# Kernel tuning notes

Hardware: AMD Instinct MI355X
Metric: run time of the kernel (lower is better)

## Reference

```python
import jax, jax.numpy as jnp
import numpy as np

CH = 128
MID = CH // 4  # 32
B, H, W = 16, 128, 128


def _phi(x):
    # elu(x) + 1 (alpha=1)
    return jax.nn.elu(x) + 1.0


def setup_inputs() -> dict:
    key = jax.random.key(0)
    ks = jax.random.split(key, 6)
    x = jax.random.normal(ks[0], (B, CH, H, W), dtype=jnp.float32)
    Wq = jax.random.normal(ks[1], (MID, CH), dtype=jnp.float32) * 0.05
    Wk = jax.random.normal(ks[2], (MID, CH), dtype=jnp.float32) * 0.05
    Wv = jax.random.normal(ks[3], (MID, CH), dtype=jnp.float32) * 0.05
    Wout = jax.random.normal(ks[4], (CH, MID), dtype=jnp.float32) * 0.05
    gamma = jnp.ones((CH,), dtype=jnp.float32)
    beta = jnp.zeros((CH,), dtype=jnp.float32)
    return {"x": x, "Wq": Wq, "Wk": Wk, "Wv": Wv, "Wout": Wout,
            "gamma": gamma, "beta": beta}


def reference(x, Wq, Wk, Wv, Wout, gamma, beta):
    b, c, h, w = x.shape
    n = h * w
    xf = x.reshape(b, c, n)                      # [B, C, N]
    # 1x1 convs == channel matmuls
    Q = _phi(jnp.einsum('mc,bcn->bmn', Wq, xf))  # [B, M, N]
    K = _phi(jnp.einsum('mc,bcn->bmn', Wk, xf))  # [B, M, N]
    V = jnp.einsum('mc,bcn->bmn', Wv, xf)        # [B, M, N]
    # KV-first linear attention
    KV = jnp.einsum('bmn,bvn->bmv', K, V)        # [B, M, M]
    out = jnp.einsum('bmv,bvn->bmn', KV, Q) / (n + 1e-6)  # [B, M, N]
    Ks = jnp.sum(K, axis=-1, keepdims=True)      # [B, M, 1]
    denom = jnp.sum(Q * Ks, axis=1, keepdims=True) + 1e-6  # [B, 1, N]
    out = out / denom
    # output 1x1 conv
    y = jnp.einsum('cm,bmn->bcn', Wout, out).reshape(b, c, h, w)
    # BatchNorm2d (training-mode forward: batch statistics, biased var, eps=1e-5)
    mean = jnp.mean(y, axis=(0, 2, 3), keepdims=True)
    var = jnp.var(y, axis=(0, 2, 3), keepdims=True)
    y = (y - mean) * jax.lax.rsqrt(var + 1e-5)
    y = y * gamma[None, :, None, None] + beta[None, :, None, None]
    return y
```

## Files before the change

### kernel.cpp

```cpp
#include <hip/hip_runtime.h>

#define BB 16
#define CC 128
#define MM 32
#define NN 16384

#define WS_KV     0
#define WS_KS     16384
#define WS_SQ     16896
#define WS_QQ     17408
#define WS_YSUM   33792
#define WS_YSQ    33920
#define WS_ACCEND 34048
#define WS_W2     34304

typedef __bf16 bf16x8 __attribute__((ext_vector_type(8)));
typedef __bf16 bf16x4 __attribute__((ext_vector_type(4)));
typedef float  f32x16 __attribute__((ext_vector_type(16)));

union B8 { bf16x8 v8; bf16x4 v4[2]; };

__device__ __forceinline__ float phi_f(float z) {
    return z > 0.f ? z + 1.f : __expf(z);
}

__device__ __forceinline__ void lds_barrier() {
    asm volatile("s_waitcnt lgkmcnt(0)" ::: "memory");
    __builtin_amdgcn_sched_barrier(0);
    __builtin_amdgcn_s_barrier();
    __builtin_amdgcn_sched_barrier(0);
}

__global__ void zero_kernel(float* ws) {
    const int i = blockIdx.x * 256 + threadIdx.x;
    if (i < (WS_ACCEND / 4)) {
        float4 z; z.x = 0.f; z.y = 0.f; z.z = 0.f; z.w = 0.f;
        ((float4*)ws)[i] = z;
    }
}

__global__ __launch_bounds__(256) void projmfma_kernel(
    const float* __restrict__ x,
    const float* __restrict__ Wq, const float* __restrict__ Wk,
    const float* __restrict__ Wv,
    float* ws, float* __restrict__ qout)
{
    __shared__ __align__(16) char smem[55296];
    __bf16* Xh  = (__bf16*)smem;
    __bf16* Xl  = (__bf16*)(smem + 17408);
    __bf16* ktH = (__bf16*)(smem + 34816);
    __bf16* ktL = (__bf16*)(smem + 39936);
    __bf16* vtH = (__bf16*)(smem + 45056);
    __bf16* vtL = (__bf16*)(smem + 50176);

    const int b = blockIdx.y;
    const int t = threadIdx.x;
    const int w = t >> 6;
    const int l = t & 63;
    const int g = l >> 5;
    const int ln31 = l & 31;

    bf16x8 wh[8], wl[8];
    if (w < 3) {
        const float* Wm = (w == 0) ? Wq : (w == 1) ? Wk : Wv;
        const float* wr = Wm + ln31 * CC;
        #pragma unroll
        for (int kt = 0; kt < 8; ++kt) {
            const int k0 = 16 * kt + 8 * g;
            #pragma unroll
            for (int j = 0; j < 8; ++j) {
                const float f = wr[k0 + j];
                const __bf16 h = (__bf16)f;
                wh[kt][j] = h;
                wl[kt][j] = (__bf16)(f - (float)h);
            }
        }
    }

    f32x16 kvA, ksA;
    bf16x8 ones;
    #pragma unroll
    for (int i = 0; i < 16; ++i) { kvA[i] = 0.f; ksA[i] = 0.f; }
    #pragma unroll
    for (int j = 0; j < 8; ++j) ones[j] = (__bf16)1.0f;

    const int px = t & 31;
    const int cb = t >> 5;

    const float* xbase = x + (size_t)b * CC * NN + (blockIdx.x << 9) + px;

    float xbuf[16];
    #pragma unroll
    for (int j = 0; j < 16; ++j)
        xbuf[j] = xbase[(size_t)(cb * 16 + j) * NN];
    {
        __bf16 hbuf[16], lbuf[16];
        #pragma unroll
        for (int j = 0; j < 16; ++j) {
            const float f = xbuf[j];
            const __bf16 h = (__bf16)f;
            hbuf[j] = h;
            lbuf[j] = (__bf16)(f - (float)h);
        }
        *(bf16x8*)&Xh[px * 136 + cb * 16]     = *(bf16x8*)&hbuf[0];
        *(bf16x8*)&Xh[px * 136 + cb * 16 + 8] = *(bf16x8*)&hbuf[8];
        *(bf16x8*)&Xl[px * 136 + cb * 16]     = *(bf16x8*)&lbuf[0];
        *(bf16x8*)&Xl[px * 136 + cb * 16 + 8] = *(bf16x8*)&lbuf[8];
    }
    lds_barrier();

    for (int tile = 0; tile < 16; ++tile) {
        const int cur = tile & 1;
        const int n0 = (blockIdx.x << 9) + (tile << 5);

        if (tile < 15) {
            const float* xp = xbase + ((tile + 1) << 5);
            #pragma unroll
            for (int j = 0; j < 16; ++j)
                xbuf[j] = xp[(size_t)(cb * 16 + j) * NN];
        }

        f32x16 acc;
        if (w < 3) {
            #pragma unroll
            for (int i = 0; i < 16; ++i) acc[i] = 0.f;
            const __bf16* xh = Xh + cur * 4352 + ln31 * 136;
            const __bf16* xl = Xl + cur * 4352 + ln31 * 136;
            #pragma unroll
            for (int kt = 0; kt < 8; ++kt) {
                const int k0 = 16 * kt + 8 * g;
                const bf16x8 bh = *(const bf16x8*)&xh[k0];
                const bf16x8 bl = *(const bf16x8*)&xl[k0];
                acc = __builtin_amdgcn_mfma_f32_32x32x16_bf16(wh[kt], bh, acc, 0, 0, 0);
                acc = __builtin_amdgcn_mfma_f32_32x32x16_bf16(wh[kt], bl, acc, 0, 0, 0);
                acc = __builtin_amdgcn_mfma_f32_32x32x16_bf16(wl[kt], bh, acc, 0, 0, 0);
            }
        } else if (tile > 0) {
            const int pbuf = (cur ^ 1) * 1280;
            const __bf16* khp = ktH + pbuf + ln31 * 40;
            const __bf16* klp = ktL + pbuf + ln31 * 40;
            const __bf16* vhp = vtH + pbuf + ln31 * 40;
            const __bf16* vlp = vtL + pbuf + ln31 * 40;
            #pragma unroll
            for (int s = 0; s < 2; ++s) {
                const int k0 = s * 16 + g * 8;
                const bf16x8 akh = *(const bf16x8*)&khp[k0];
                const bf16x8 akl = *(const bf16x8*)&klp[k0];
                const bf16x8 bvh = *(const bf16x8*)&vhp[k0];
                const bf16x8 bvl = *(const bf16x8*)&vlp[k0];
                kvA = __builtin_amdgcn_mfma_f32_32x32x16_bf16(akh, bvh, kvA, 0, 0, 0);
                kvA = __builtin_amdgcn_mfma_f32_32x32x16_bf16(akh, bvl, kvA, 0, 0, 0);
                kvA = __builtin_amdgcn_mfma_f32_32x32x16_bf16(akl, bvh, kvA, 0, 0, 0);
                ksA = __builtin_amdgcn_mfma_f32_32x32x16_bf16(akh, ones, ksA, 0, 0, 0);
                ksA = __builtin_amdgcn_mfma_f32_32x32x16_bf16(akl, ones, ksA, 0, 0, 0);
            }
        }

        if (w == 0) {
            float* qp = qout + (size_t)b * CC * NN + n0 + ln31;
            #pragma unroll
            for (int i = 0; i < 16; ++i) {
                const int r = (i & 3) + 8 * (i >> 2) + 4 * g;
                qp[(size_t)r * NN] = phi_f(acc[i]);
            }
        } else if (w == 1) {
            __bf16* kh = ktH + cur * 1280;
            __bf16* kl = ktL + cur * 1280;
            #pragma unroll
            for (int i = 0; i < 16; ++i) {
                const int r = (i & 3) + 8 * (i >> 2) + 4 * g;
                const float f = phi_f(acc[i]);
                const __bf16 h = (__bf16)f;
                kh[r * 40 + ln31] = h;
                kl[r * 40 + ln31] = (__bf16)(f - (float)h);
            }
        } else if (w == 2) {
            __bf16* vh = vtH + cur * 1280;
            __bf16* vl = vtL + cur * 1280;
            #pragma unroll
            for (int i = 0; i < 16; ++i) {
                const int r = (i & 3) + 8 * (i >> 2) + 4 * g;
                const float f = acc[i];
                const __bf16 h = (__bf16)f;
                vh[r * 40 + ln31] = h;
                vl[r * 40 + ln31] = (__bf16)(f - (float)h);
            }
        }

        if (tile < 15) {
            const int nxt = cur ^ 1;
            __bf16 hbuf[16], lbuf[16];
            #pragma unroll
            for (int j = 0; j < 16; ++j) {
                const float f = xbuf[j];
                const __bf16 h = (__bf16)f;
                hbuf[j] = h;
                lbuf[j] = (__bf16)(f - (float)h);
            }
            *(bf16x8*)&Xh[nxt * 4352 + px * 136 + cb * 16]     = *(bf16x8*)&hbuf[0];
            *(bf16x8*)&Xh[nxt * 4352 + px * 136 + cb * 16 + 8] = *(bf16x8*)&hbuf[8];
            *(bf16x8*)&Xl[nxt * 4352 + px * 136 + cb * 16]     = *(bf16x8*)&lbuf[0];
            *(bf16x8*)&Xl[nxt * 4352 + px * 136 + cb * 16 + 8] = *(bf16x8*)&lbuf[8];
        }

        lds_barrier();
    }

    if (w == 3) {
        const int pbuf = 1280;
        const __bf16* khp = ktH + pbuf + ln31 * 40;
        const __bf16* klp = ktL + pbuf + ln31 * 40;
        const __bf16* vhp = vtH + pbuf + ln31 * 40;
        const __bf16* vlp = vtL + pbuf + ln31 * 40;
        #pragma unroll
        for (int s = 0; s < 2; ++s) {
            const int k0 = s * 16 + g * 8;
            const bf16x8 akh = *(const bf16x8*)&khp[k0];
            const bf16x8 akl = *(const bf16x8*)&klp[k0];
            const bf16x8 bvh = *(const bf16x8*)&vhp[k0];
            const bf16x8 bvl = *(const bf16x8*)&vlp[k0];
            kvA = __builtin_amdgcn_mfma_f32_32x32x16_bf16(akh, bvh, kvA, 0, 0, 0);
            kvA = __builtin_amdgcn_mfma_f32_32x32x16_bf16(akh, bvl, kvA, 0, 0, 0);
            kvA = __builtin_amdgcn_mfma_f32_32x32x16_bf16(akl, bvh, kvA, 0, 0, 0);
            ksA = __builtin_amdgcn_mfma_f32_32x32x16_bf16(akh, ones, ksA, 0, 0, 0);
            ksA = __builtin_amdgcn_mfma_f32_32x32x16_bf16(akl, ones, ksA, 0, 0, 0);
        }
        float* kvb = ws + WS_KV + (b << 10);
        #pragma unroll
        for (int i = 0; i < 16; ++i) {
            const int r = (i & 3) + 8 * (i >> 2) + 4 * g;
            atomicAdd(&kvb[r * 32 + ln31], kvA[i]);
        }
        if (ln31 == 0) {
            #pragma unroll
            for (int i = 0; i < 16; ++i) {
                const int r = (i & 3) + 8 * (i >> 2) + 4 * g;
                atomicAdd(&ws[WS_KS + (b << 5) + r], ksA[i]);
            }
        }
    }
}

__global__ __launch_bounds__(256) void qq_kernel(const float* qsrc, float* ws) {
    __shared__ __align__(16) char qsm[33792];
    __bf16* Qh = (__bf16*)qsm;
    __bf16* Ql = (__bf16*)(qsm + 16896);
    float*  red   = (float*)qsm;
    float*  sqred = (float*)(qsm + 17408);

    const int b = blockIdx.y;
    const int t = threadIdx.x;
    const int w = t >> 6;
    const int l = t & 63;
    const int g = l >> 5;
    const int ln31 = l & 31;

    const float* ksb = ws + WS_KS + (b << 5);
    const int n = (blockIdx.x << 8) + t;
    const float* qp = qsrc + (size_t)b * CC * NN + n;

    float qa[32];
    #pragma unroll
    for (int m = 0; m < 32; ++m) qa[m] = qp[(size_t)m * NN];

    float denom = 1e-6f;
    #pragma unroll
    for (int m = 0; m < 32; ++m) denom = fmaf(qa[m], ksb[m], denom);
    const float inv = 1.0f / (16384.0f * denom);
    #pragma unroll
    for (int m = 0; m < 32; ++m) qa[m] *= inv;

    #pragma unroll
    for (int m = 0; m < 32; ++m) {
        const __bf16 h = (__bf16)qa[m];
        Qh[m * 264 + t] = h;
        Ql[m * 264 + t] = (__bf16)(qa[m] - (float)h);
    }
    __syncthreads();

    f32x16 qqA, sqA;
    bf16x8 ones;
    #pragma unroll
    for (int i = 0; i < 16; ++i) { qqA[i] = 0.f; sqA[i] = 0.f; }
    #pragma unroll
    for (int j = 0; j < 8; ++j) ones[j] = (__bf16)1.0f;

    #pragma unroll
    for (int sub = 0; sub < 2; ++sub) {
        #pragma unroll
        for (int s = 0; s < 2; ++s) {
            const int k0 = (w << 6) + (sub << 5) + s * 16 + g * 8;
            const bf16x8 ah = *(const bf16x8*)&Qh[ln31 * 264 + k0];
            const bf16x8 al = *(const bf16x8*)&Ql[ln31 * 264 + k0];
            qqA = __builtin_amdgcn_mfma_f32_32x32x16_bf16(ah, ah, qqA, 0, 0, 0);
            qqA = __builtin_amdgcn_mfma_f32_32x32x16_bf16(ah, al, qqA, 0, 0, 0);
            qqA = __builtin_amdgcn_mfma_f32_32x32x16_bf16(al, ah, qqA, 0, 0, 0);
            sqA = __builtin_amdgcn_mfma_f32_32x32x16_bf16(ah, ones, sqA, 0, 0, 0);
            sqA = __builtin_amdgcn_mfma_f32_32x32x16_bf16(al, ones, sqA, 0, 0, 0);
        }
    }
    __syncthreads();

    #pragma unroll
    for (int i = 0; i < 16; ++i) red[t * 17 + i] = qqA[i];
    if (ln31 == 0) {
        #pragma unroll
        for (int i = 0; i < 16; ++i) {
            const int r = (i & 3) + 8 * (i >> 2) + 4 * g;
            sqred[(w << 5) + r] = sqA[i];
        }
    }
    __syncthreads();
    if (t < 64) {
        float* qqb = ws + WS_QQ + (b << 10);
        #pragma unroll
        for (int i = 0; i < 16; ++i) {
            const int r = (i & 3) + 8 * (i >> 2) + 4 * g;
            const float s = red[t*17+i] + red[(t+64)*17+i] + red[(t+128)*17+i] + red[(t+192)*17+i];
            atomicAdd(&qqb[r * 32 + ln31], s);
        }
    }
    if (t < 32) {
        const float s = sqred[t] + sqred[32 + t] + sqred[64 + t] + sqred[96 + t];
        atomicAdd(&ws[WS_SQ + (b << 5) + t], s);
    }
}

__global__ __launch_bounds__(128) void bnstat_kernel(const float* __restrict__ Wout,
                                                     float* ws) {
    const int b = blockIdx.x;
    const int c = threadIdx.x;
    const float* kvb = ws + WS_KV + (b << 10);
    const float* wo  = Wout + (c << 5);
    float w[32];
    #pragma unroll
    for (int v = 0; v < 32; ++v) w[v] = 0.f;
    for (int m = 0; m < 32; ++m) {
        const float wm = wo[m];
        #pragma unroll
        for (int v = 0; v < 32; ++v) w[v] = fmaf(wm, kvb[(m << 5) + v], w[v]);
    }
    float* w2b = ws + WS_W2 + (b << 12) + (c << 5);
    #pragma unroll
    for (int v = 0; v < 32; ++v) w2b[v] = w[v];

    const float* sq = ws + WS_SQ + (b << 5);
    const float* qq = ws + WS_QQ + (b << 10);
    float mb = 0.f;
    #pragma unroll
    for (int v = 0; v < 32; ++v) mb = fmaf(w[v], sq[v], mb);
    float qf = 0.f;
    for (int u = 0; u < 32; ++u) {
        float tacc = 0.f;
        #pragma unroll
        for (int v = 0; v < 32; ++v) tacc = fmaf(qq[(u << 5) + v], w[v], tacc);
        qf = fmaf(w[u], tacc, qf);
    }
    atomicAdd(&ws[WS_YSUM + c], mb);
    atomicAdd(&ws[WS_YSQ + c], qf);
}

__global__ __launch_bounds__(256) void out_kernel(const float* qsrc, const float* ws,
                                                  const float* __restrict__ gamma,
                                                  const float* __restrict__ beta,
                                                  float* out) {
    __shared__ __align__(16) __bf16 Qh[256 * 36];
    __shared__ __align__(16) __bf16 Ql[256 * 36];
    __shared__ float scs[CC];
    __shared__ float bis[CC];

    const int b = blockIdx.y;
    const int t = threadIdx.x;
    const int w = t >> 6;
    const int l = t & 63;
    const int g = l >> 5;
    const int ln31 = l & 31;

    if (t < CC) {
        const float invBN = 1.0f / 262144.0f;
        const float mean = ws[WS_YSUM + t] * invBN;
        const float var  = ws[WS_YSQ + t] * invBN - mean * mean;
        const float s = gamma[t] * rsqrtf(var + 1e-5f);
        scs[t] = s;
        bis[t] = fmaf(-mean, s, beta[t]);
    }

    const int n = (blockIdx.x << 8) + t;
    const float* ksb = ws + WS_KS + (b << 5);

    const float* qp = qsrc + (size_t)b * CC * NN + n;
    float qa[32];
    #pragma unroll
    for (int m = 0; m < 32; ++m) qa[m] = qp[(size_t)m * NN];

    float d0 = 1e-6f;
    #pragma unroll
    for (int m = 0; m < 32; ++m) d0 = fmaf(qa[m], ksb[m], d0);
    const float inv = 1.0f / (16384.0f * d0);
    #pragma unroll
    for (int m = 0; m < 32; ++m) qa[m] *= inv;

    {
        __bf16 qh[32], ql[32];
        #pragma unroll
        for (int m = 0; m < 32; ++m) {
            const __bf16 h = (__bf16)qa[m];
            qh[m] = h;
            ql[m] = (__bf16)(qa[m] - (float)h);
        }
        #pragma unroll
        for (int i = 0; i < 8; ++i) {
            *(bf16x4*)&Qh[t * 36 + i * 4] = *(bf16x4*)&qh[i * 4];
            *(bf16x4*)&Ql[t * 36 + i * 4] = *(bf16x4*)&ql[i * 4];
        }
    }
    __syncthreads();

    const float* w2b = ws + WS_W2 + (b << 12);
    float* ob = out + (size_t)b * CC * NN + (blockIdx.x << 8);

    #pragma unroll
    for (int cb = 0; cb < 4; ++cb) {
        bf16x8 ah[2], al[2];
        #pragma unroll
        for (int kt = 0; kt < 2; ++kt) {
            const float* wp = w2b + (cb * 32 + ln31) * 32 + kt * 16 + g * 8;
            #pragma unroll
            for (int j = 0; j < 8; ++j) {
                const float f = wp[j];
                const __bf16 h = (__bf16)f;
                ah[kt][j] = h;
                al[kt][j] = (__bf16)(f - (float)h);
            }
        }
        #pragma unroll
        for (int pg = 0; pg < 2; ++pg) {
            const int px0 = (w << 6) + (pg << 5);
            f32x16 acc;
            #pragma unroll
            for (int i = 0; i < 16; ++i) acc[i] = 0.f;
            #pragma unroll
            for (int kt = 0; kt < 2; ++kt) {
                const int k0 = kt * 16 + g * 8;
                const __bf16* qhp = &Qh[(px0 + ln31) * 36 + k0];
                const __bf16* qlp = &Ql[(px0 + ln31) * 36 + k0];
                B8 bh, bl;
                bh.v4[0] = *(const bf16x4*)&qhp[0];
                bh.v4[1] = *(const bf16x4*)&qhp[4];
                bl.v4[0] = *(const bf16x4*)&qlp[0];
                bl.v4[1] = *(const bf16x4*)&qlp[4];
                acc = __builtin_amdgcn_mfma_f32_32x32x16_bf16(ah[kt], bh.v8, acc, 0, 0, 0);
                acc = __builtin_amdgcn_mfma_f32_32x32x16_bf16(ah[kt], bl.v8, acc, 0, 0, 0);
                acc = __builtin_amdgcn_mfma_f32_32x32x16_bf16(al[kt], bh.v8, acc, 0, 0, 0);
            }
            #pragma unroll
            for (int i = 0; i < 16; ++i) {
                const int r = (i & 3) + 8 * (i >> 2) + 4 * g;
                const int c = cb * 32 + r;
                const float v = fmaf(scs[c], acc[i], bis[c]);
                __builtin_nontemporal_store(v, &ob[(size_t)c * NN + px0 + ln31]);
            }
        }
    }
}

extern "C" void kernel_launch(void* const* d_in, const int* in_sizes, int n_in,
                              void* d_out, int out_size, void* d_ws, size_t ws_size,
                              hipStream_t stream) {
    const float* x     = (const float*)d_in[0];
    const float* Wq    = (const float*)d_in[1];
    const float* Wk    = (const float*)d_in[2];
    const float* Wv    = (const float*)d_in[3];
    const float* Wout  = (const float*)d_in[4];
    const float* gamma = (const float*)d_in[5];
    const float* beta  = (const float*)d_in[6];
    float* ws  = (float*)d_ws;
    float* out = (float*)d_out;

    zero_kernel<<<34, 256, 0, stream>>>(ws);
    projmfma_kernel<<<dim3(32, 16), 256, 0, stream>>>(x, Wq, Wk, Wv, ws, out);
    qq_kernel<<<dim3(64, 16), 256, 0, stream>>>(out, ws);
    bnstat_kernel<<<16, 128, 0, stream>>>(Wout, ws);
    out_kernel<<<dim3(64, 16), 256, 0, stream>>>(out, ws, gamma, beta, out);
}
```

Measured before the change: 114.0 us.

## Drop x low-part split, widen projection tile to 64 pixels

The projection kernel stops splitting x into bf16 high and low parts and keeps only the high part, going from three MFMAs per k-step to two per output tile. The pixel tile grows from 32 to 64, so each wave runs two accumulators and the loop runs 8 iterations instead of 16. The register prefetch of the next x tile is removed: loads now happen at the top of each iteration, followed by a barrier. This cuts MFMA work, LDS traffic and conversion work, but loses precision on x, exposes global load latency, and raises LDS use to 70 KB, which may reduce occupancy.

New measurement: 110.8 us, median of 2. 1.03x faster.

```diff
diff --git a/kernel.cpp b/kernel.cpp
--- a/kernel.cpp
+++ b/kernel.cpp
@@ -45,13 +45,12 @@
     const float* __restrict__ Wv,
     float* ws, float* __restrict__ qout)
 {
-    __shared__ __align__(16) char smem[55296];
+    __shared__ __align__(16) char smem[71680];
     __bf16* Xh  = (__bf16*)smem;
-    __bf16* Xl  = (__bf16*)(smem + 17408);
     __bf16* ktH = (__bf16*)(smem + 34816);
-    __bf16* ktL = (__bf16*)(smem + 39936);
-    __bf16* vtH = (__bf16*)(smem + 45056);
-    __bf16* vtL = (__bf16*)(smem + 50176);
+    __bf16* ktL = (__bf16*)(smem + 44032);
+    __bf16* vtH = (__bf16*)(smem + 53248);
+    __bf16* vtL = (__bf16*)(smem + 62464);
 
     const int b = blockIdx.y;
     const int t = threadIdx.x;
@@ -84,65 +83,93 @@
     #pragma unroll
     for (int j = 0; j < 8; ++j) ones[j] = (__bf16)1.0f;
 
-    const int px = t & 31;
-    const int cb = t >> 5;
+    const int px = t & 63;
+    const int cb = t >> 6;
 
     const float* xbase = x + (size_t)b * CC * NN + (blockIdx.x << 9) + px;
 
-    float xbuf[16];
-    #pragma unroll
-    for (int j = 0; j < 16; ++j)
-        xbuf[j] = xbase[(size_t)(cb * 16 + j) * NN];
-    {
-        __bf16 hbuf[16], lbuf[16];
-        #pragma unroll
-        for (int j = 0; j < 16; ++j) {
-            const float f = xbuf[j];
-            const __bf16 h = (__bf16)f;
-            hbuf[j] = h;
-            lbuf[j] = (__bf16)(f - (float)h);
-        }
-        *(bf16x8*)&Xh[px * 136 + cb * 16]     = *(bf16x8*)&hbuf[0];
-        *(bf16x8*)&Xh[px * 136 + cb * 16 + 8] = *(bf16x8*)&hbuf[8];
-        *(bf16x8*)&Xl[px * 136 + cb * 16]     = *(bf16x8*)&lbuf[0];
-        *(bf16x8*)&Xl[px * 136 + cb * 16 + 8] = *(bf16x8*)&lbuf[8];
-    }
-    lds_barrier();
-
-    for (int tile = 0; tile < 16; ++tile) {
+    for (int tile = 0; tile < 8; ++tile) {
         const int cur = tile & 1;
-        const int n0 = (blockIdx.x << 9) + (tile << 5);
-
-        if (tile < 15) {
-            const float* xp = xbase + ((tile + 1) << 5);
-            #pragma unroll
-            for (int j = 0; j < 16; ++j)
-                xbuf[j] = xp[(size_t)(cb * 16 + j) * NN];
-        }
-
-        f32x16 acc;
+        const int n0 = (blockIdx.x << 9) + (tile << 6);
+
+        {
+            const float* xp = xbase + (tile << 6);
+            float xb[32];
+            #pragma unroll
+            for (int j = 0; j < 32; ++j)
+                xb[j] = xp[(size_t)(cb * 32 + j) * NN];
+            __bf16 hb[32];
+            #pragma unroll
+            for (int j = 0; j < 32; ++j) hb[j] = (__bf16)xb[j];
+            #pragma unroll
+            for (int q = 0; q < 4; ++q)
+                *(bf16x8*)&Xh[cur * 8704 + px * 136 + cb * 32 + q * 8] =
+                    *(bf16x8*)&hb[q * 8];
+        }
+        lds_barrier();
+
         if (w < 3) {
-            #pragma unroll
-            for (int i = 0; i < 16; ++i) acc[i] = 0.f;
-            const __bf16* xh = Xh + cur * 4352 + ln31 * 136;
-            const __bf16* xl = Xl + cur * 4352 + ln31 * 136;
+            f32x16 a0, a1;
+            #pragma unroll
+            for (int i = 0; i < 16; ++i) { a0[i] = 0.f; a1[i] = 0.f; }
+            const __bf16* xh = Xh + cur * 8704;
             #pragma unroll
             for (int kt = 0; kt < 8; ++kt) {
                 const int k0 = 16 * kt + 8 * g;
-                const bf16x8 bh = *(const bf16x8*)&xh[k0];
-                const bf16x8 bl = *(const bf16x8*)&xl[k0];
-                acc = __builtin_amdgcn_mfma_f32_32x32x16_bf16(wh[kt], bh, acc, 0, 0, 0);
-                acc = __builtin_amdgcn_mfma_f32_32x32x16_bf16(wh[kt], bl, acc, 0, 0, 0);
-                acc = __builtin_amdgcn_mfma_f32_32x32x16_bf16(wl[kt], bh, acc, 0, 0, 0);
+                const bf16x8 b0 = *(const bf16x8*)&xh[ln31 * 136 + k0];
+                const bf16x8 b1 = *(const bf16x8*)&xh[(ln31 + 32) * 136 + k0];
+                a0 = __builtin_amdgcn_mfma_f32_32x32x16_bf16(wh[kt], b0, a0, 0, 0, 0);
+                a0 = __builtin_amdgcn_mfma_f32_32x32x16_bf16(wl[kt], b0, a0, 0, 0, 0);
+                a1 = __builtin_amdgcn_mfma_f32_32x32x16_bf16(wh[kt], b1, a1, 0, 0, 0);
+                a1 = __builtin_amdgcn_mfma_f32_32x32x16_bf16(wl[kt], b1, a1, 0, 0, 0);
+            }
+            if (w == 0) {
+                float* qp = qout + (size_t)b * CC * NN + n0 + ln31;
+                #pragma unroll
+                for (int i = 0; i < 16; ++i) {
+                    const int r = (i & 3) + 8 * (i >> 2) + 4 * g;
+                    qp[(size_t)r * NN]      = phi_f(a0[i]);
+                    qp[(size_t)r * NN + 32] = phi_f(a1[i]);
+                }
+            } else if (w == 1) {
+                __bf16* kh = ktH + cur * 2304;
+                __bf16* kl = ktL + cur * 2304;
+                #pragma unroll
+                for (int i = 0; i < 16; ++i) {
+                    const int r = (i & 3) + 8 * (i >> 2) + 4 * g;
+                    const float f0 = phi_f(a0[i]);
+                    const float f1 = phi_f(a1[i]);
+                    const __bf16 h0 = (__bf16)f0;
+                    const __bf16 h1 = (__bf16)f1;
+                    kh[r * 72 + ln31]      = h0;
+                    kl[r * 72 + ln31]      = (__bf16)(f0 - (float)h0);
+                    kh[r * 72 + 32 + ln31] = h1;
+                    kl[r * 72 + 32 + ln31] = (__bf16)(f1 - (float)h1);
+                }
+            } else {
+                __bf16* vh = vtH + cur * 2304;
+                __bf16* vl = vtL + cur * 2304;
+                #pragma unroll
+                for (int i = 0; i < 16; ++i) {
+                    const int r = (i & 3) + 8 * (i >> 2) + 4 * g;
+                    const float f0 = a0[i];
+                    const float f1 = a1[i];
+                    const __bf16 h0 = (__bf16)f0;
+                    const __bf16 h1 = (__bf16)f1;
+                    vh[r * 72 + ln31]      = h0;
+                    vl[r * 72 + ln31]      = (__bf16)(f0 - (float)h0);
+                    vh[r * 72 + 32 + ln31] = h1;
+                    vl[r * 72 + 32 + ln31] = (__bf16)(f1 - (float)h1);
+                }
             }
         } else if (tile > 0) {
-            const int pbuf = (cur ^ 1) * 1280;
-            const __bf16* khp = ktH + pbuf + ln31 * 40;
-            const __bf16* klp = ktL + pbuf + ln31 * 40;
-            const __bf16* vhp = vtH + pbuf + ln31 * 40;
-            const __bf16* vlp = vtL + pbuf + ln31 * 40;
-            #pragma unroll
-            for (int s = 0; s < 2; ++s) {
+            const int pb = (cur ^ 1) * 2304;
+            const __bf16* khp = ktH + pb + ln31 * 72;
+            const __bf16* klp = ktL + pb + ln31 * 72;
+            const __bf16* vhp = vtH + pb + ln31 * 72;
+            const __bf16* vlp = vtL + pb + ln31 * 72;
+            #pragma unroll
+            for (int s = 0; s < 4; ++s) {
                 const int k0 = s * 16 + g * 8;
                 const bf16x8 akh = *(const bf16x8*)&khp[k0];
                 const bf16x8 akl = *(const bf16x8*)&klp[k0];
@@ -155,65 +182,17 @@
                 ksA = __builtin_amdgcn_mfma_f32_32x32x16_bf16(akl, ones, ksA, 0, 0, 0);
             }
         }
-
-        if (w == 0) {
-            float* qp = qout + (size_t)b * CC * NN + n0 + ln31;
-            #pragma unroll
-            for (int i = 0; i < 16; ++i) {
-                const int r = (i & 3) + 8 * (i >> 2) + 4 * g;
-                qp[(size_t)r * NN] = phi_f(acc[i]);
-            }
-        } else if (w == 1) {
-            __bf16* kh = ktH + cur * 1280;
-            __bf16* kl = ktL + cur * 1280;
-            #pragma unroll
-            for (int i = 0; i < 16; ++i) {
-                const int r = (i & 3) + 8 * (i >> 2) + 4 * g;
-                const float f = phi_f(acc[i]);
-                const __bf16 h = (__bf16)f;
-                kh[r * 40 + ln31] = h;
-                kl[r * 40 + ln31] = (__bf16)(f - (float)h);
-            }
-        } else if (w == 2) {
-            __bf16* vh = vtH + cur * 1280;
-            __bf16* vl = vtL + cur * 1280;
-            #pragma unroll
-            for (int i = 0; i < 16; ++i) {
-                const int r = (i & 3) + 8 * (i >> 2) + 4 * g;
-                const float f = acc[i];
-                const __bf16 h = (__bf16)f;
-                vh[r * 40 + ln31] = h;
-                vl[r * 40 + ln31] = (__bf16)(f - (float)h);
-            }
-        }
-
-        if (tile < 15) {
-            const int nxt = cur ^ 1;
-            __bf16 hbuf[16], lbuf[16];
-            #pragma unroll
-            for (int j = 0; j < 16; ++j) {
-                const float f = xbuf[j];
-                const __bf16 h = (__bf16)f;
-                hbuf[j] = h;
-                lbuf[j] = (__bf16)(f - (float)h);
-            }
-            *(bf16x8*)&Xh[nxt * 4352 + px * 136 + cb * 16]     = *(bf16x8*)&hbuf[0];
-            *(bf16x8*)&Xh[nxt * 4352 + px * 136 + cb * 16 + 8] = *(bf16x8*)&hbuf[8];
-            *(bf16x8*)&Xl[nxt * 4352 + px * 136 + cb * 16]     = *(bf16x8*)&lbuf[0];
-            *(bf16x8*)&Xl[nxt * 4352 + px * 136 + cb * 16 + 8] = *(bf16x8*)&lbuf[8];
-        }
-
         lds_barrier();
     }
 
     if (w == 3) {
-        const int pbuf = 1280;
-        const __bf16* khp = ktH + pbuf + ln31 * 40;
-        const __bf16* klp = ktL + pbuf + ln31 * 40;
-        const __bf16* vhp = vtH + pbuf + ln31 * 40;
-        const __bf16* vlp = vtL + pbuf + ln31 * 40;
-        #pragma unroll
-        for (int s = 0; s < 2; ++s) {
+        const int pb = 2304;
+        const __bf16* khp = ktH + pb + ln31 * 72;
+        const __bf16* klp = ktL + pb + ln31 * 72;
+        const __bf16* vhp = vtH + pb + ln31 * 72;
+        const __bf16* vlp = vtL + pb + ln31 * 72;
+        #pragma unroll
+        for (int s = 0; s < 4; ++s) {
             const int k0 = s * 16 + g * 8;
             const bf16x8 akh = *(const bf16x8*)&khp[k0];
             const bf16x8 akl = *(const bf16x8*)&klp[k0];
```

## Pre-pack x into transposed bf16 layout and weights into split bf16 in workspace

Applied to the files above, without the earlier changes.

Adds a separate kernel that transposes x into a pixel-major bf16 (high part only) buffer stored in the output scratch, and a kernel that pre-splits the projection weights into bf16 high/low pairs. The projection kernel then reads MFMA operands directly from global memory without LDS staging and drops the x-low correction term, using two MFMAs per k-step instead of three, with twice as many blocks. This trades an extra read/write pass over x and two more launches for lower LDS pressure and higher occupancy, and lowers the precision of the x operand.

Measured after the change: 177.5 us. 1.56x slower.

```diff
diff --git a/kernel.cpp b/kernel.cpp
--- a/kernel.cpp
+++ b/kernel.cpp
@@ -13,10 +13,12 @@
 #define WS_YSQ    33920
 #define WS_ACCEND 34048
 #define WS_W2     34304
+#define WS_WPACK  99840
 
 typedef __bf16 bf16x8 __attribute__((ext_vector_type(8)));
 typedef __bf16 bf16x4 __attribute__((ext_vector_type(4)));
 typedef float  f32x16 __attribute__((ext_vector_type(16)));
+typedef unsigned short ushort4v __attribute__((ext_vector_type(4)));
 
 union B8 { bf16x8 v8; bf16x4 v4[2]; };
 
@@ -31,6 +33,11 @@
     __builtin_amdgcn_sched_barrier(0);
 }
 
+__device__ __forceinline__ unsigned short bf16bits(float f) {
+    const __bf16 h = (__bf16)f;
+    return __builtin_bit_cast(unsigned short, h);
+}
+
 __global__ void zero_kernel(float* ws) {
     const int i = blockIdx.x * 256 + threadIdx.x;
     if (i < (WS_ACCEND / 4)) {
@@ -39,19 +46,68 @@
     }
 }
 
+__global__ void wpack_kernel(const float* __restrict__ Wq,
+                             const float* __restrict__ Wk,
+                             const float* __restrict__ Wv, float* ws) {
+    __bf16* wp = (__bf16*)(ws + WS_WPACK);
+    const int idx = blockIdx.x * 256 + threadIdx.x;
+    if (idx < 12288) {
+        const int mi  = idx >> 12;
+        const int rem = idx & 4095;
+        const float f = (mi == 0 ? Wq : mi == 1 ? Wk : Wv)[rem];
+        const __bf16 h = (__bf16)f;
+        wp[idx]         = h;
+        wp[12288 + idx] = (__bf16)(f - (float)h);
+    }
+}
+
+__global__ __launch_bounds__(256) void xpack_kernel(const float* __restrict__ x,
+                                                    float* out) {
+    __shared__ unsigned short tile[128 * 260];
+    const int b = blockIdx.y;
+    const int slab = blockIdx.x;
+    const int t = threadIdx.x;
+    unsigned short* xT = (unsigned short*)(out + (size_t)b * CC * NN + (size_t)32 * NN);
+
+    for (int st = 0; st < 2; ++st) {
+        const int n0 = slab * 512 + st * 256;
+        if (st) __syncthreads();
+        const int l = t & 63;
+        #pragma unroll 4
+        for (int cc = 0; cc < 32; ++cc) {
+            const int c = cc * 4 + (t >> 6);
+            const float4 v = ((const float4*)(x + (size_t)b * CC * NN
+                                              + (size_t)c * NN + n0))[l];
+            ushort4v hv;
+            hv[0] = bf16bits(v.x); hv[1] = bf16bits(v.y);
+            hv[2] = bf16bits(v.z); hv[3] = bf16bits(v.w);
+            *(ushort4v*)&tile[c * 260 + 4 * l] = hv;
+        }
+        __syncthreads();
+        uint4* dst = (uint4*)(xT + (size_t)(n0 + t) * 128);
+        #pragma unroll
+        for (int ci = 0; ci < 16; ++ci) {
+            unsigned int u[4];
+            #pragma unroll
+            for (int q = 0; q < 4; ++q) {
+                const unsigned int lo = tile[(ci * 8 + 2 * q) * 260 + t];
+                const unsigned int hi = tile[(ci * 8 + 2 * q + 1) * 260 + t];
+                u[q] = lo | (hi << 16);
+            }
+            uint4 vv; vv.x = u[0]; vv.y = u[1]; vv.z = u[2]; vv.w = u[3];
+            dst[ci] = vv;
+        }
+    }
+}
+
 __global__ __launch_bounds__(256) void projmfma_kernel(
-    const float* __restrict__ x,
-    const float* __restrict__ Wq, const float* __restrict__ Wk,
-    const float* __restrict__ Wv,
-    float* ws, float* __restrict__ qout)
+    const float* ws_c, float* ws, float* out)
 {
-    __shared__ __align__(16) char smem[55296];
-    __bf16* Xh  = (__bf16*)smem;
-    __bf16* Xl  = (__bf16*)(smem + 17408);
-    __bf16* ktH = (__bf16*)(smem + 34816);
-    __bf16* ktL = (__bf16*)(smem + 39936);
-    __bf16* vtH = (__bf16*)(smem + 45056);
-    __bf16* vtL = (__bf16*)(smem + 50176);
+    __shared__ __align__(16) char smem[20480];
+    __bf16* ktH = (__bf16*)smem;
+    __bf16* ktL = (__bf16*)(smem + 5120);
+    __bf16* vtH = (__bf16*)(smem + 10240);
+    __bf16* vtL = (__bf16*)(smem + 15360);
 
     const int b = blockIdx.y;
     const int t = threadIdx.x;
@@ -62,18 +118,11 @@
 
     bf16x8 wh[8], wl[8];
     if (w < 3) {
-        const float* Wm = (w == 0) ? Wq : (w == 1) ? Wk : Wv;
-        const float* wr = Wm + ln31 * CC;
+        const __bf16* wp = (const __bf16*)(ws_c + WS_WPACK) + w * 4096 + ln31 * 128;
         #pragma unroll
         for (int kt = 0; kt < 8; ++kt) {
-            const int k0 = 16 * kt + 8 * g;
-            #pragma unroll
-            for (int j = 0; j < 8; ++j) {
-                const float f = wr[k0 + j];
-                const __bf16 h = (__bf16)f;
-                wh[kt][j] = h;
-                wl[kt][j] = (__bf16)(f - (float)h);
-            }
+            wh[kt] = *(const bf16x8*)&wp[16 * kt + 8 * g];
+            wl[kt] = *(const bf16x8*)&wp[12288 + 16 * kt + 8 * g];
         }
     }
 
@@ -84,56 +133,55 @@
     #pragma unroll
     for (int j = 0; j < 8; ++j) ones[j] = (__bf16)1.0f;
 
-    const int px = t & 31;
-    const int cb = t >> 5;
-
-    const float* xbase = x + (size_t)b * CC * NN + (blockIdx.x << 9) + px;
-
-    float xbuf[16];
-    #pragma unroll
-    for (int j = 0; j < 16; ++j)
-        xbuf[j] = xbase[(size_t)(cb * 16 + j) * NN];
-    {
-        __bf16 hbuf[16], lbuf[16];
-        #pragma unroll
-        for (int j = 0; j < 16; ++j) {
-            const float f = xbuf[j];
-            const __bf16 h = (__bf16)f;
-            hbuf[j] = h;
-            lbuf[j] = (__bf16)(f - (float)h);
-        }
-        *(bf16x8*)&Xh[px * 136 + cb * 16]     = *(bf16x8*)&hbuf[0];
-        *(bf16x8*)&Xh[px * 136 + cb * 16 + 8] = *(bf16x8*)&hbuf[8];
-        *(bf16x8*)&Xl[px * 136 + cb * 16]     = *(bf16x8*)&lbuf[0];
-        *(bf16x8*)&Xl[px * 136 + cb * 16 + 8] = *(bf16x8*)&lbuf[8];
-    }
-    lds_barrier();
-
-    for (int tile = 0; tile < 16; ++tile) {
+    const __bf16* xT = (const __bf16*)((const float*)out + (size_t)b * CC * NN
+                                       + (size_t)32 * NN);
+    float* qout = out + (size_t)b * CC * NN;
+    const int pxbase = blockIdx.x << 8;
+
+    for (int tile = 0; tile < 8; ++tile) {
         const int cur = tile & 1;
-        const int n0 = (blockIdx.x << 9) + (tile << 5);
-
-        if (tile < 15) {
-            const float* xp = xbase + ((tile + 1) << 5);
-            #pragma unroll
-            for (int j = 0; j < 16; ++j)
-                xbuf[j] = xp[(size_t)(cb * 16 + j) * NN];
-        }
-
-        f32x16 acc;
+        const int n0 = pxbase + (tile << 5);
+
         if (w < 3) {
+            f32x16 acc;
             #pragma unroll
             for (int i = 0; i < 16; ++i) acc[i] = 0.f;
-            const __bf16* xh = Xh + cur * 4352 + ln31 * 136;
-            const __bf16* xl = Xl + cur * 4352 + ln31 * 136;
+            const __bf16* xp = xT + (size_t)(n0 + ln31) * 128;
             #pragma unroll
             for (int kt = 0; kt < 8; ++kt) {
-                const int k0 = 16 * kt + 8 * g;
-                const bf16x8 bh = *(const bf16x8*)&xh[k0];
-                const bf16x8 bl = *(const bf16x8*)&xl[k0];
+                const bf16x8 bh = *(const bf16x8*)&xp[16 * kt + 8 * g];
                 acc = __builtin_amdgcn_mfma_f32_32x32x16_bf16(wh[kt], bh, acc, 0, 0, 0);
-                acc = __builtin_amdgcn_mfma_f32_32x32x16_bf16(wh[kt], bl, acc, 0, 0, 0);
                 acc = __builtin_amdgcn_mfma_f32_32x32x16_bf16(wl[kt], bh, acc, 0, 0, 0);
+            }
+            if (w == 0) {
+                float* qp = qout + n0 + ln31;
+                #pragma unroll
+                for (int i = 0; i < 16; ++i) {
+                    const int r = (i & 3) + 8 * (i >> 2) + 4 * g;
+                    qp[(size_t)r * NN] = phi_f(acc[i]);
+                }
+            } else if (w == 1) {
+                __bf16* kh = ktH + cur * 1280;
+                __bf16* kl = ktL + cur * 1280;
+                #pragma unroll
+                for (int i = 0; i < 16; ++i) {
+                    const int r = (i & 3) + 8 * (i >> 2) + 4 * g;
+                    const float f = phi_f(acc[i]);
+                    const __bf16 h = (__bf16)f;
+                    kh[r * 40 + ln31] = h;
+                    kl[r * 40 + ln31] = (__bf16)(f - (float)h);
+                }
+            } else {
+                __bf16* vh = vtH + cur * 1280;
+                __bf16* vl = vtL + cur * 1280;
+                #pragma unroll
+                for (int i = 0; i < 16; ++i) {
+                    const int r = (i & 3) + 8 * (i >> 2) + 4 * g;
+                    const float f = acc[i];
+                    const __bf16 h = (__bf16)f;
+                    vh[r * 40 + ln31] = h;
+                    vl[r * 40 + ln31] = (__bf16)(f - (float)h);
+                }
             }
         } else if (tile > 0) {
             const int pbuf = (cur ^ 1) * 1280;
@@ -155,54 +203,6 @@
                 ksA = __builtin_amdgcn_mfma_f32_32x32x16_bf16(akl, ones, ksA, 0, 0, 0);
             }
         }
-
-        if (w == 0) {
-            float* qp = qout + (size_t)b * CC * NN + n0 + ln31;
-            #pragma unroll
-            for (int i = 0; i < 16; ++i) {
-                const int r = (i & 3) + 8 * (i >> 2) + 4 * g;
-                qp[(size_t)r * NN] = phi_f(acc[i]);
-            }
-        } else if (w == 1) {
-            __bf16* kh = ktH + cur * 1280;
-            __bf16* kl = ktL + cur * 1280;
-            #pragma unroll
-            for (int i = 0; i < 16; ++i) {
-                const int r = (i & 3) + 8 * (i >> 2) + 4 * g;
-                const float f = phi_f(acc[i]);
-                const __bf16 h = (__bf16)f;
-                kh[r * 40 + ln31] = h;
-                kl[r * 40 + ln31] = (__bf16)(f - (float)h);
-            }
-        } else if (w == 2) {
-            __bf16* vh = vtH + cur * 1280;
-            __bf16* vl = vtL + cur * 1280;
-            #pragma unroll
-            for (int i = 0; i < 16; ++i) {
-                const int r = (i & 3) + 8 * (i >> 2) + 4 * g;
-                const float f = acc[i];
-                const __bf16 h = (__bf16)f;
-                vh[r * 40 + ln31] = h;
-                vl[r * 40 + ln31] = (__bf16)(f - (float)h);
-            }
-        }
-
-        if (tile < 15) {
-            const int nxt = cur ^ 1;
-            __bf16 hbuf[16], lbuf[16];
-            #pragma unroll
-            for (int j = 0; j < 16; ++j) {
-                const float f = xbuf[j];
-                const __bf16 h = (__bf16)f;
-                hbuf[j] = h;
-                lbuf[j] = (__bf16)(f - (float)h);
-            }
-            *(bf16x8*)&Xh[nxt * 4352 + px * 136 + cb * 16]     = *(bf16x8*)&hbuf[0];
-            *(bf16x8*)&Xh[nxt * 4352 + px * 136 + cb * 16 + 8] = *(bf16x8*)&hbuf[8];
-            *(bf16x8*)&Xl[nxt * 4352 + px * 136 + cb * 16]     = *(bf16x8*)&lbuf[0];
-            *(bf16x8*)&Xl[nxt * 4352 + px * 136 + cb * 16 + 8] = *(bf16x8*)&lbuf[8];
-        }
-
         lds_barrier();
     }
 
@@ -478,7 +478,9 @@
     float* out = (float*)d_out;
 
     zero_kernel<<<34, 256, 0, stream>>>(ws);
-    projmfma_kernel<<<dim3(32, 16), 256, 0, stream>>>(x, Wq, Wk, Wv, ws, out);
+    wpack_kernel<<<48, 256, 0, stream>>>(Wq, Wk, Wv, ws);
+    xpack_kernel<<<dim3(32, 16), 256, 0, stream>>>(x, out);
+    projmfma_kernel<<<dim3(64, 16), 256, 0, stream>>>(ws, ws, out);
     qq_kernel<<<dim3(64, 16), 256, 0, stream>>>(out, ws);
     bnstat_kernel<<<16, 128, 0, stream>>>(Wout, ws);
     out_kernel<<<dim3(64, 16), 256, 0, stream>>>(out, ws, gamma, beta, out);
```
